# Optimization experiments

Measured on AMD Instinct MI355X. Metric: run time of the kernel, lower is better.

## Reference

```python
import jax, jax.numpy as jnp
import numpy as np

IN_F = 1024
OUT_F = 1024

def setup_inputs() -> dict:
    key = jax.random.key(0)
    ks = jax.random.split(key, 7)
    s = 1.0 / np.sqrt(IN_F)
    x = jax.random.normal(ks[0], (4, 2048, IN_F), dtype=jnp.float32)
    Wq = jax.random.uniform(ks[1], (OUT_F, IN_F), jnp.float32, -s, s)
    bq = jax.random.uniform(ks[2], (OUT_F,), jnp.float32, -s, s)
    Wk = jax.random.uniform(ks[3], (OUT_F, IN_F), jnp.float32, -s, s)
    bk = jax.random.uniform(ks[4], (OUT_F,), jnp.float32, -s, s)
    Wv = jax.random.uniform(ks[5], (OUT_F, IN_F), jnp.float32, -s, s)
    bv = jax.random.uniform(ks[6], (OUT_F,), jnp.float32, -s, s)
    return {"x": x, "Wq": Wq, "bq": bq, "Wk": Wk, "bk": bk, "Wv": Wv, "bv": bv}

def reference(x, Wq, bq, Wk, bk, Wv, bv):
    # Projector: ReLU(Linear(x))
    q = jax.nn.relu(jnp.einsum('bsd,od->bso', x, Wq) + bq)  # [B,S,O]
    k = jax.nn.relu(jnp.einsum('bsd,od->bso', x, Wk) + bk)
    v = jax.nn.relu(jnp.einsum('bsd,od->bso', x, Wv) + bv)
    logits = jnp.einsum('bio,bko->bik', q, k)  # unscaled QK^T, [B,S,S]
    scores = jax.nn.softmax(logits, axis=-1)
    out = jnp.einsum('bik,bko->bio', scores, v)
    return out
```

## Files before the change

kernel.cpp:

```cpp
#include <hip/hip_runtime.h>
#include <hip/hip_bf16.h>


#define SEQ 2048
#define DIM 1024
#define NB 4
#define MTOT (NB * SEQ)

typedef __attribute__((ext_vector_type(8))) short frag_ab;
typedef __attribute__((ext_vector_type(16))) float frag_c16;

__device__ __forceinline__ ushort f2bf(float f) {
    union { float f; unsigned u; } x; x.f = f;
    unsigned r = x.u + 0x7fffu + ((x.u >> 16) & 1u);
    return (ushort)(r >> 16);
}

typedef __attribute__((address_space(1))) const unsigned int guint;
typedef __attribute__((address_space(3))) unsigned int luint;

__device__ __forceinline__ void gld_lds16(const void* g, void* l) {
    __builtin_amdgcn_global_load_lds((guint*)g, (luint*)l, 16, 0, 0);
}

__device__ __forceinline__ void bar() {
    asm volatile("" ::: "memory");
    __builtin_amdgcn_s_barrier();
    asm volatile("" ::: "memory");
}
#define VMCNT(n) asm volatile("s_waitcnt vmcnt(" #n ")" ::: "memory")

#define TB (128 * 32)

__device__ __forceinline__ void gemm_tiles(
    const ushort* __restrict__ A, size_t lda,
    const ushort* __restrict__ B, size_t ldb, int K,
    ushort* As, ushort* Bs, frag_c16 (&acc)[2][2])
{
    const int tid  = threadIdx.x;
    const int wave = tid >> 6;
    const int lane = tid & 63;
    const int l32  = lane & 31;
    const int half = lane >> 5;
    const int sr = wave * 16 + (lane >> 2);
    const int sc = lane & 3;
    const int wm = (wave & 1) * 64;
    const int wn = (wave >> 1) * 64;
    const int nkt = K >> 5;

    #define STAGE_TILE(kt, b) do {                                          \
        int k0_ = (kt) << 5;                                                \
        _Pragma("unroll")                                                   \
        for (int j = 0; j < 2; ++j) {                                       \
            int row = j * 64 + sr;                                          \
            int cg  = sc ^ ((row >> 1) & 3);                                \
            ushort* la = As + (b) * TB + (j * 64 + wave * 16) * 32;         \
            ushort* lb = Bs + (b) * TB + (j * 64 + wave * 16) * 32;         \
            gld_lds16(A + (size_t)row * lda + k0_ + cg * 8, la);            \
            gld_lds16(B + (size_t)row * ldb + k0_ + cg * 8, lb);            \
        }                                                                   \
    } while (0)

    STAGE_TILE(0, 0);
    for (int t = 0; t < nkt; ++t) {
        const int c = t & 1;
        int tn = t + 1 < nkt ? t + 1 : nkt - 1;
        STAGE_TILE(tn, c ^ 1);
        VMCNT(4);
        bar();

        const ushort* Ac = As + c * TB;
        const ushort* Bc = Bs + c * TB;
        frag_ab af[2][2], bfr[2][2];
        #pragma unroll
        for (int mi = 0; mi < 2; ++mi) {
            int row = wm + mi * 32 + l32;
            int sw = (row >> 1) & 3;
            #pragma unroll
            for (int h = 0; h < 2; ++h) {
                int cc = (h * 2 + half) ^ sw;
                af[mi][h] = *(const frag_ab*)&Ac[row * 32 + cc * 8];
            }
        }
        #pragma unroll
        for (int ni = 0; ni < 2; ++ni) {
            int row = wn + ni * 32 + l32;
            int sw = (row >> 1) & 3;
            #pragma unroll
            for (int h = 0; h < 2; ++h) {
                int cc = (h * 2 + half) ^ sw;
                bfr[ni][h] = *(const frag_ab*)&Bc[row * 32 + cc * 8];
            }
        }
        asm volatile("s_waitcnt lgkmcnt(0)" ::: "memory");
        __builtin_amdgcn_sched_barrier(0);
        bar();

        #pragma unroll
        for (int h = 0; h < 2; ++h)
            #pragma unroll
            for (int mi = 0; mi < 2; ++mi)
                #pragma unroll
                for (int ni = 0; ni < 2; ++ni)
                    acc[mi][ni] = __builtin_amdgcn_mfma_f32_32x32x16_bf16(
                        af[mi][h], bfr[ni][h], acc[mi][ni], 0, 0, 0);
    }
    VMCNT(0);
    #undef STAGE_TILE
}


#define NX4 (MTOT * DIM / 4)
#define NW4 (DIM * DIM / 4)
__global__ __launch_bounds__(256) void cvt_kernel(
    const float* __restrict__ x,
    const float* __restrict__ Wq, const float* __restrict__ Wk,
    const float* __restrict__ Wv,
    ushort* __restrict__ xb, ushort* __restrict__ Wb)
{
    size_t i = (size_t)blockIdx.x * 256 + threadIdx.x;
    const float* src; ushort* dst; size_t idx;
    if (i < NX4) { src = x; dst = xb; idx = i; }
    else {
        size_t j = i - NX4;
        int w = (int)(j >> 18);
        idx = j & (NW4 - 1);
        src = w == 0 ? Wq : (w == 1 ? Wk : Wv);
        dst = Wb + (size_t)w * DIM * DIM;
    }
    float4 f = ((const float4*)src)[idx];
    ushort4 u; u.x = f2bf(f.x); u.y = f2bf(f.y); u.z = f2bf(f.z); u.w = f2bf(f.w);
    ((ushort4*)dst)[idx] = u;
}

__global__ __launch_bounds__(256) void qkv_kernel(
    const ushort* __restrict__ xb, const ushort* __restrict__ Wb,
    const float* __restrict__ bq, const float* __restrict__ bk,
    const float* __restrict__ bv,
    ushort* __restrict__ q, ushort* __restrict__ kk, ushort* __restrict__ vt)
{
    const float* bias;
    if (blockIdx.z == 0)      bias = bq;
    else if (blockIdx.z == 1) bias = bk;
    else                      bias = bv;
    const ushort* W = Wb + (size_t)blockIdx.z * DIM * DIM;

    __shared__ ushort As[2 * TB];
    __shared__ ushort Bs[2 * TB];

    const int tid  = threadIdx.x;
    const int wave = tid >> 6;
    const int lane = tid & 63;
    const int l32  = lane & 31;
    const int half = lane >> 5;
    const int m0 = blockIdx.x * 128;
    const int n0 = blockIdx.y * 128;
    const int wm = (wave & 1) * 64;
    const int wn = (wave >> 1) * 64;

    frag_c16 acc[2][2] = {};
    gemm_tiles(xb + (size_t)m0 * DIM, DIM, W + (size_t)n0 * DIM, DIM, DIM,
               As, Bs, acc);

    if (blockIdx.z == 2) {
        const int bz = m0 >> 11;
        const int sb = (m0 & (SEQ - 1)) + wm;
        #pragma unroll
        for (int ni = 0; ni < 2; ++ni) {
            int col = n0 + wn + ni * 32 + l32;
            float bb = bias[col];
            ushort* vrow = vt + ((size_t)(bz * DIM + col)) * SEQ;
            #pragma unroll
            for (int mi = 0; mi < 2; ++mi)
                #pragma unroll
                for (int g = 0; g < 4; ++g) {
                    int s0 = sb + mi * 32 + 8 * g + 4 * half;
                    ushort4 u;
                    #pragma unroll
                    for (int j = 0; j < 4; ++j) {
                        float val = acc[mi][ni][4 * g + j] + bb;
                        val = val > 0.0f ? val : 0.0f;
                        ((ushort*)&u)[j] = f2bf(val);
                    }
                    *(ushort4*)&vrow[s0] = u;
                }
        }
    } else {
        ushort* out = blockIdx.z == 0 ? q : kk;
        #pragma unroll
        for (int ni = 0; ni < 2; ++ni) {
            int col = n0 + wn + ni * 32 + l32;
            float bb = bias[col];
            #pragma unroll
            for (int mi = 0; mi < 2; ++mi)
                #pragma unroll
                for (int r = 0; r < 16; ++r) {
                    int row = m0 + wm + mi * 32 + (r & 3) + 8 * (r >> 2) + 4 * half;
                    float val = acc[mi][ni][r] + bb;
                    val = val > 0.0f ? val : 0.0f;
                    out[(size_t)row * DIM + col] = f2bf(val);
                }
        }
    }
}

__global__ __launch_bounds__(256) void qk_kernel(
    const ushort* __restrict__ q, const ushort* __restrict__ kk,
    float* __restrict__ logits)
{
    __shared__ ushort As[2 * TB];
    __shared__ ushort Bs[2 * TB];

    const int tid  = threadIdx.x;
    const int wave = tid >> 6;
    const int lane = tid & 63;
    const int l32  = lane & 31;
    const int half = lane >> 5;
    const int bz = blockIdx.z;
    const int m0 = blockIdx.x * 128;
    const int n0 = blockIdx.y * 128;
    const int wm = (wave & 1) * 64;
    const int wn = (wave >> 1) * 64;
    const size_t base = (size_t)bz * SEQ;

    frag_c16 acc[2][2] = {};
    gemm_tiles(q + (base + m0) * DIM, DIM, kk + (base + n0) * DIM, DIM, DIM,
               As, Bs, acc);

    #pragma unroll
    for (int mi = 0; mi < 2; ++mi)
        #pragma unroll
        for (int r = 0; r < 16; ++r) {
            int row = m0 + wm + mi * 32 + (r & 3) + 8 * (r >> 2) + 4 * half;
            #pragma unroll
            for (int ni = 0; ni < 2; ++ni) {
                int col = n0 + wn + ni * 32 + l32;
                logits[(base + row) * SEQ + col] = acc[mi][ni][r];
            }
        }
}

__global__ __launch_bounds__(256) void softmax_kernel(float* __restrict__ logits)
{
    const int row  = blockIdx.x * 4 + (threadIdx.x >> 6);
    const int lane = threadIdx.x & 63;
    float* p = logits + (size_t)row * SEQ;

    float4 x[8];
    #pragma unroll
    for (int i = 0; i < 8; ++i) x[i] = ((const float4*)p)[lane + 64 * i];

    float m = -3.4e38f;
    #pragma unroll
    for (int i = 0; i < 8; ++i)
        m = fmaxf(m, fmaxf(fmaxf(x[i].x, x[i].y), fmaxf(x[i].z, x[i].w)));
    #pragma unroll
    for (int off = 32; off; off >>= 1) m = fmaxf(m, __shfl_xor(m, off, 64));

    float s = 0.0f;
    #pragma unroll
    for (int i = 0; i < 8; ++i) {
        x[i].x = __expf(x[i].x - m); x[i].y = __expf(x[i].y - m);
        x[i].z = __expf(x[i].z - m); x[i].w = __expf(x[i].w - m);
        s += (x[i].x + x[i].y) + (x[i].z + x[i].w);
    }
    #pragma unroll
    for (int off = 32; off; off >>= 1) s += __shfl_xor(s, off, 64);
    float inv = 1.0f / s;

    ushort* o = (ushort*)p;
    #pragma unroll
    for (int i = 0; i < 8; ++i) {
        ushort4 u;
        u.x = f2bf(x[i].x * inv); u.y = f2bf(x[i].y * inv);
        u.z = f2bf(x[i].z * inv); u.w = f2bf(x[i].w * inv);
        ((ushort4*)o)[lane + 64 * i] = u;
    }
}

__global__ __launch_bounds__(256) void pv_kernel(
    const ushort* __restrict__ probs, const ushort* __restrict__ vt,
    float* __restrict__ out)
{
    __shared__ ushort As[2 * TB];
    __shared__ ushort Bs[2 * TB];

    const int tid  = threadIdx.x;
    const int wave = tid >> 6;
    const int lane = tid & 63;
    const int l32  = lane & 31;
    const int half = lane >> 5;
    const int bz = blockIdx.z;
    const int m0 = blockIdx.x * 128;
    const int n0 = blockIdx.y * 128;
    const int wm = (wave & 1) * 64;
    const int wn = (wave >> 1) * 64;

    frag_c16 acc[2][2] = {};
    gemm_tiles(probs + ((size_t)(bz * SEQ + m0)) * 4096, 4096,
               vt + ((size_t)(bz * DIM + n0)) * SEQ, SEQ, SEQ,
               As, Bs, acc);

    #pragma unroll
    for (int mi = 0; mi < 2; ++mi)
        #pragma unroll
        for (int r = 0; r < 16; ++r) {
            int row = m0 + wm + mi * 32 + (r & 3) + 8 * (r >> 2) + 4 * half;
            #pragma unroll
            for (int ni = 0; ni < 2; ++ni) {
                int col = n0 + wn + ni * 32 + l32;
                out[((size_t)(bz * SEQ + row)) * DIM + col] = acc[mi][ni][r];
            }
        }
}

extern "C" void kernel_launch(void* const* d_in, const int* in_sizes, int n_in,
                              void* d_out, int out_size, void* d_ws, size_t ws_size,
                              hipStream_t stream)
{
    const float* x  = (const float*)d_in[0];
    const float* Wq = (const float*)d_in[1];
    const float* bq = (const float*)d_in[2];
    const float* Wk = (const float*)d_in[3];
    const float* bk = (const float*)d_in[4];
    const float* Wv = (const float*)d_in[5];
    const float* bv = (const float*)d_in[6];
    float* out = (float*)d_out;

    char* ws = (char*)d_ws;
    ushort* q      = (ushort*)(ws);
    ushort* kk     = (ushort*)(ws + ((size_t)16 << 20));
    ushort* vt     = (ushort*)(ws + ((size_t)48 << 20));
    float*  logits = (float*) (ws + ((size_t)64 << 20));
    ushort* xb     = (ushort*)(ws + ((size_t)64 << 20));
    ushort* Wb     = (ushort*)(ws + ((size_t)80 << 20));

    cvt_kernel<<<dim3((NX4 + 3 * NW4) / 256), 256, 0, stream>>>(
        x, Wq, Wk, Wv, xb, Wb);

    qkv_kernel<<<dim3(MTOT / 128, DIM / 128, 3), 256, 0, stream>>>(
        xb, Wb, bq, bk, bv, q, kk, vt);
    qk_kernel<<<dim3(SEQ / 128, SEQ / 128, NB), 256, 0, stream>>>(q, kk, logits);
    softmax_kernel<<<NB * SEQ / 4, 256, 0, stream>>>(logits);
    pv_kernel<<<dim3(SEQ / 128, DIM / 128, NB), 256, 0, stream>>>(
        (const ushort*)logits, vt, out);
}
```

Baseline: 292.5 us.

## Double K-tile depth to 64 with 8-way XOR swizzle and barrier after MFMAs

Raises the per-iteration K slice of the shared GEMM routine from 32 to 64, doubling the LDS tile size. Staging is rewritten to load 8-row groups with an XOR swizzle over 8 column chunks, and fragments are read as four K-steps. The mid-iteration barrier after the LDS reads is replaced by one barrier at the end of the loop. The aim is to halve the number of barriers and K iterations per output tile, at the cost of more LDS and registers, which may reduce occupancy.

```diff
diff --git a/kernel.cpp b/kernel.cpp
--- a/kernel.cpp
+++ b/kernel.cpp
@@ -30,7 +30,7 @@
 }
 #define VMCNT(n) asm volatile("s_waitcnt vmcnt(" #n ")" ::: "memory")
 
-#define TB (128 * 32)
+#define TB (128 * 64)
 
 __device__ __forceinline__ void gemm_tiles(
     const ushort* __restrict__ A, size_t lda,
@@ -42,22 +42,23 @@
     const int lane = tid & 63;
     const int l32  = lane & 31;
     const int half = lane >> 5;
-    const int sr = wave * 16 + (lane >> 2);
-    const int sc = lane & 3;
+    const int rin  = lane >> 3;
+    const int cp   = lane & 7;
+    const int cl   = cp ^ rin;
     const int wm = (wave & 1) * 64;
     const int wn = (wave >> 1) * 64;
-    const int nkt = K >> 5;
+    const int nkt = K >> 6;
 
     #define STAGE_TILE(kt, b) do {                                          \
-        int k0_ = (kt) << 5;                                                \
+        int k0_ = (kt) << 6;                                                \
         _Pragma("unroll")                                                   \
-        for (int j = 0; j < 2; ++j) {                                       \
-            int row = j * 64 + sr;                                          \
-            int cg  = sc ^ ((row >> 1) & 3);                                \
-            ushort* la = As + (b) * TB + (j * 64 + wave * 16) * 32;         \
-            ushort* lb = Bs + (b) * TB + (j * 64 + wave * 16) * 32;         \
-            gld_lds16(A + (size_t)row * lda + k0_ + cg * 8, la);            \
-            gld_lds16(B + (size_t)row * ldb + k0_ + cg * 8, lb);            \
+        for (int g = 0; g < 4; ++g) {                                       \
+            int qc  = g * 4 + wave;                                         \
+            int row = qc * 8 + rin;                       \
+            gld_lds16(A + (size_t)row * lda + k0_ + cl * 8,                 \
+                      As + (b) * TB + qc * 512);                            \
+            gld_lds16(B + (size_t)row * ldb + k0_ + cl * 8,                 \
+                      Bs + (b) * TB + qc * 512);                            \
         }                                                                   \
     } while (0)
 
@@ -66,44 +67,41 @@
         const int c = t & 1;
         int tn = t + 1 < nkt ? t + 1 : nkt - 1;
         STAGE_TILE(tn, c ^ 1);
-        VMCNT(4);
+        VMCNT(8);
         bar();
 
         const ushort* Ac = As + c * TB;
         const ushort* Bc = Bs + c * TB;
-        frag_ab af[2][2], bfr[2][2];
+        frag_ab af[2][4], bf[2][4];
         #pragma unroll
         for (int mi = 0; mi < 2; ++mi) {
             int row = wm + mi * 32 + l32;
-            int sw = (row >> 1) & 3;
-            #pragma unroll
-            for (int h = 0; h < 2; ++h) {
-                int cc = (h * 2 + half) ^ sw;
-                af[mi][h] = *(const frag_ab*)&Ac[row * 32 + cc * 8];
+            int sw = row & 7;
+            #pragma unroll
+            for (int ks = 0; ks < 4; ++ks) {
+                int cc = (ks * 2 + half) ^ sw;
+                af[mi][ks] = *(const frag_ab*)&Ac[row * 64 + cc * 8];
             }
         }
         #pragma unroll
         for (int ni = 0; ni < 2; ++ni) {
             int row = wn + ni * 32 + l32;
-            int sw = (row >> 1) & 3;
-            #pragma unroll
-            for (int h = 0; h < 2; ++h) {
-                int cc = (h * 2 + half) ^ sw;
-                bfr[ni][h] = *(const frag_ab*)&Bc[row * 32 + cc * 8];
+            int sw = row & 7;
+            #pragma unroll
+            for (int ks = 0; ks < 4; ++ks) {
+                int cc = (ks * 2 + half) ^ sw;
+                bf[ni][ks] = *(const frag_ab*)&Bc[row * 64 + cc * 8];
             }
         }
-        asm volatile("s_waitcnt lgkmcnt(0)" ::: "memory");
-        __builtin_amdgcn_sched_barrier(0);
-        bar();
-
-        #pragma unroll
-        for (int h = 0; h < 2; ++h)
+        #pragma unroll
+        for (int ks = 0; ks < 4; ++ks)
             #pragma unroll
             for (int mi = 0; mi < 2; ++mi)
                 #pragma unroll
                 for (int ni = 0; ni < 2; ++ni)
                     acc[mi][ni] = __builtin_amdgcn_mfma_f32_32x32x16_bf16(
-                        af[mi][h], bfr[ni][h], acc[mi][ni], 0, 0, 0);
+                        af[mi][ks], bf[ni][ks], acc[mi][ni], 0, 0, 0);
+        bar();
     }
     VMCNT(0);
     #undef STAGE_TILE
```

New measurement: 262.3 us. 1.12x faster.
